# Performance work log

Hardware: AMD Instinct MI355X
Metric: run time of the kernel (lower is better)

The kernel has to match this reference:

```python
import jax, jax.numpy as jnp
import numpy as np

NUM_CLASSES = 80
ROI_SIZE = 7
SAMPLING = 2          # RoIAlign sampling_ratio
STRIDES = (4, 8, 16, 32)
FINEST_SCALE = 56.0
SCORE_THR = 0.05
IOU_THR = 0.5
MAX_PER_IMG = 100
MEANS = jnp.zeros((4,), jnp.float32)
STDS = jnp.array([0.1, 0.1, 0.2, 0.2], jnp.float32)
MAX_RATIO = abs(float(np.log(16.0 / 1000.0)))


def setup_inputs() -> dict:
    key = jax.random.key(0)
    ks = jax.random.split(key, 20)
    C, H0, W0 = 256, 200, 336
    inp = {}
    for i in range(4):
        inp[f"feat{i}"] = jax.random.normal(ks[i], (1, C, H0 >> i, W0 >> i), jnp.float32)
    N = 1000
    IMG_W, IMG_H = 1344.0, 800.0
    cx = jax.random.uniform(ks[4], (N,), minval=0.0, maxval=IMG_W)
    cy = jax.random.uniform(ks[5], (N,), minval=0.0, maxval=IMG_H)
    w = jax.random.uniform(ks[6], (N,), minval=16.0, maxval=512.0)
    h = jax.random.uniform(ks[7], (N,), minval=16.0, maxval=512.0)
    x1 = jnp.clip(cx - w / 2, 0.0, IMG_W - 1)
    y1 = jnp.clip(cy - h / 2, 0.0, IMG_H - 1)
    x2 = jnp.clip(cx + w / 2, x1 + 1.0, IMG_W)
    y2 = jnp.clip(cy + h / 2, y1 + 1.0, IMG_H)
    inp["proposals"] = jnp.stack([x1, y1, x2, y2], axis=-1)
    D = C * ROI_SIZE * ROI_SIZE  # 12544
    FC = 1024
    inp["fc1_w"] = 0.01 * jax.random.normal(ks[8], (FC, D), jnp.float32)
    inp["fc1_b"] = jnp.zeros((FC,), jnp.float32)
    inp["fc2_w"] = 0.01 * jax.random.normal(ks[9], (FC, FC), jnp.float32)
    inp["fc2_b"] = jnp.zeros((FC,), jnp.float32)
    inp["cls_w"] = 0.01 * jax.random.normal(ks[10], (NUM_CLASSES + 1, FC), jnp.float32)
    inp["cls_b"] = jnp.zeros((NUM_CLASSES + 1,), jnp.float32)
    inp["reg_w"] = 0.01 * jax.random.normal(ks[11], (NUM_CLASSES * 4, FC), jnp.float32)
    inp["reg_b"] = jnp.zeros((NUM_CLASSES * 4,), jnp.float32)
    return inp


def _roi_align(feat, rois, scale):
    # feat [C,H,W]; rois [N,4]; aligned RoIAlign, 7x7 out, sampling_ratio=2
    C, H, W = feat.shape
    P = ROI_SIZE * SAMPLING  # 14 uniform sample points per axis

    def one(roi):
        x1, y1, x2, y2 = roi[0], roi[1], roi[2], roi[3]
        sx = x1 * scale - 0.5
        sy = y1 * scale - 0.5
        rw = (x2 - x1) * scale
        rh = (y2 - y1) * scale
        pts = (jnp.arange(P, dtype=feat.dtype) + 0.5) / P
        xs = sx + pts * rw
        ys = sy + pts * rh
        y0 = jnp.floor(ys)
        x0 = jnp.floor(xs)
        ly = ys - y0
        lx = xs - x0
        y0i = jnp.clip(y0.astype(jnp.int32), 0, H - 1)
        y1i = jnp.clip(y0i + 1, 0, H - 1)
        x0i = jnp.clip(x0.astype(jnp.int32), 0, W - 1)
        x1i = jnp.clip(x0i + 1, 0, W - 1)
        g = lambda yi, xi: feat[:, yi[:, None], xi[None, :]]  # [C,P,P]
        ly_ = ly[None, :, None]
        lx_ = lx[None, None, :]
        val = (1 - ly_) * ((1 - lx_) * g(y0i, x0i) + lx_ * g(y0i, x1i)) \
            + ly_ * ((1 - lx_) * g(y1i, x0i) + lx_ * g(y1i, x1i))
        vy = ((ys >= -1.0) & (ys <= H))[None, :, None]
        vx = ((xs >= -1.0) & (xs <= W))[None, None, :]
        val = jnp.where(vy & vx, val, 0.0)
        # average-pool the 2x2 samples per bin -> [C,7,7]
        return val.reshape(C, ROI_SIZE, SAMPLING, ROI_SIZE, SAMPLING).mean(axis=(2, 4))

    return jax.vmap(one)(rois)  # [N,C,7,7]


def _delta2bbox(proposals, deltas):
    d = deltas.reshape(-1, NUM_CLASSES, 4) * STDS + MEANS
    dx, dy = d[..., 0], d[..., 1]
    dw = jnp.clip(d[..., 2], -MAX_RATIO, MAX_RATIO)
    dh = jnp.clip(d[..., 3], -MAX_RATIO, MAX_RATIO)
    px = ((proposals[:, 0] + proposals[:, 2]) * 0.5)[:, None]
    py = ((proposals[:, 1] + proposals[:, 3]) * 0.5)[:, None]
    pw = (proposals[:, 2] - proposals[:, 0])[:, None]
    ph = (proposals[:, 3] - proposals[:, 1])[:, None]
    gw = pw * jnp.exp(dw)
    gh = ph * jnp.exp(dh)
    gx = px + pw * dx
    gy = py + ph * dy
    return jnp.stack([gx - gw * 0.5, gy - gh * 0.5, gx + gw * 0.5, gy + gh * 0.5], axis=-1)


def _pairwise_iou(b):
    x1, y1, x2, y2 = b[:, 0], b[:, 1], b[:, 2], b[:, 3]
    area = jnp.maximum(x2 - x1, 0.0) * jnp.maximum(y2 - y1, 0.0)
    iw = jnp.maximum(jnp.minimum(x2[:, None], x2[None, :]) - jnp.maximum(x1[:, None], x1[None, :]), 0.0)
    ih = jnp.maximum(jnp.minimum(y2[:, None], y2[None, :]) - jnp.maximum(y1[:, None], y1[None, :]), 0.0)
    inter = iw * ih
    return inter / jnp.maximum(area[:, None] + area[None, :] - inter, 1e-8)


def _nms_one_class(boxes, scores):
    # greedy NMS, static shapes; returns score-sorted boxes/scores + keep mask
    N = scores.shape[0]
    order = jnp.argsort(-scores)
    b = boxes[order]
    s = scores[order]
    iou = _pairwise_iou(b)
    idx = jnp.arange(N)

    def body(i, keep):
        sup = (iou[i] > IOU_THR) & keep[i] & (idx > i)
        return keep & jnp.logical_not(sup)

    keep = jax.lax.fori_loop(0, N, body, s > SCORE_THR)
    return b, s, keep


def _batched_nms(bboxes, scores):
    # bboxes [N,81,4], scores [N,81]; class 80 is background (skipped)
    cls_boxes = jnp.transpose(bboxes[:, :NUM_CLASSES, :], (1, 0, 2))  # [80,N,4]
    cls_scores = scores[:, :NUM_CLASSES].T                            # [80,N]
    b, s, keep = jax.vmap(_nms_one_class)(cls_boxes, cls_scores)
    N = s.shape[1]
    s_flat = jnp.where(keep, s, -1.0).reshape(-1)
    topv, topi = jax.lax.top_k(s_flat, MAX_PER_IMG)
    det_boxes = b.reshape(-1, 4)[topi]
    det_classes = (topi // N).astype(jnp.int32)
    valid = topv > 0.0
    num_det = valid.sum().astype(jnp.int32)
    det_scores = jnp.where(valid, topv, 0.0)
    det_boxes = jnp.where(valid[:, None], det_boxes, 0.0)
    det_classes = jnp.where(valid, det_classes, -1)
    return num_det, det_boxes[None], det_scores[None], det_classes[None]


def _forward(feat0, feat1, feat2, feat3, proposals,
             fc1_w, fc1_b, fc2_w, fc2_b, cls_w, cls_b, reg_w, reg_b):
    feats = [feat0[0], feat1[0], feat2[0], feat3[0]]
    wp = proposals[:, 2] - proposals[:, 0]
    hp = proposals[:, 3] - proposals[:, 1]
    scale = jnp.sqrt(jnp.maximum(wp * hp, 1e-6))
    lvl = jnp.clip(jnp.floor(jnp.log2(scale / FINEST_SCALE + 1e-6)), 0, 3).astype(jnp.int32)
    N = proposals.shape[0]
    C = feats[0].shape[0]
    roi_feats = jnp.zeros((N, C, ROI_SIZE, ROI_SIZE), proposals.dtype)
    for l, stride in enumerate(STRIDES):
        f = _roi_align(feats[l], proposals, 1.0 / stride)
        roi_feats = jnp.where((lvl == l)[:, None, None, None], f, roi_feats)
    h = roi_feats.reshape(N, -1)
    h = jax.nn.relu(h @ fc1_w.T + fc1_b)
    h = jax.nn.relu(h @ fc2_w.T + fc2_b)
    cls_score = h @ cls_w.T + cls_b          # [N,81]
    bbox_pred = h @ reg_w.T + reg_b          # [N,320]
    scores = jax.nn.softmax(cls_score, axis=1)
    boxes = _delta2bbox(proposals, bbox_pred)                          # [N,80,4]
    boxes = jnp.concatenate([boxes, jnp.zeros((N, 1, 4), boxes.dtype)], axis=1)
    return _batched_nms(boxes, scores)


def reference(feat0, feat1, feat2, feat3, proposals,
              fc1_w, fc1_b, fc2_w, fc2_b, cls_w, cls_b, reg_w, reg_b):
    return _forward(feat0, feat1, feat2, feat3, proposals,
                    fc1_w, fc1_b, fc2_w, fc2_b, cls_w, cls_b, reg_w, reg_b)
```

## Files before the change

kernel.cpp:

```cpp
#include <hip/hip_runtime.h>
#include <math.h>

#define NCLS   80
#define NPROP  1000
#define FCDIM  1024
#define DFLAT  12544
#define MPAD   1024
#define MAXR   4.1351665567423560f
#define LDSP   40
#define NMSW   16
#define NCAT   404

#define CSPLIT 8
#define CG     (256 / CSPLIT)

typedef unsigned short ushort_t;
typedef unsigned long long ull_t;
using short8  = __attribute__((ext_vector_type(8))) short;
using float4v = __attribute__((ext_vector_type(4))) float;

__device__ inline ushort_t f2bf(float f) {
    unsigned int u = __float_as_uint(f);
    unsigned int r = (u + 0x7fffu + ((u >> 16) & 1u)) >> 16;
    return (ushort_t)r;
}

__device__ __forceinline__ unsigned cvtpk_bf16(float lo, float hi) {
    unsigned r;
    asm("v_cvt_pk_bf16_f32 %0, %1, %2" : "=v"(r) : "v"(lo), "v"(hi));
    return r;
}

__global__ __launch_bounds__(256) void roi_align_k(
    const float* __restrict__ f0, const float* __restrict__ f1,
    const float* __restrict__ f2, const float* __restrict__ f3,
    const float* __restrict__ props, ushort_t* __restrict__ Abf)
{
    int r  = blockIdx.x;
    int cz = blockIdx.y;
    int t  = threadIdx.x;

    if (r >= NPROP) {
        for (int i = t; i < CG * 49; i += 256)
            Abf[(size_t)r * DFLAT + cz * (CG * 49) + i] = 0;
        return;
    }

    const float4 p = *(const float4*)&props[(size_t)r * 4];
    float wp = p.z - p.x, hp = p.w - p.y;
    float scale = sqrtf(fmaxf(wp * hp, 1e-6f));
    int lvl = (int)floorf(log2f(scale / 56.0f + 1e-6f));
    lvl = min(max(lvl, 0), 3);

    const float* f; int H, W; float sc;
    switch (lvl) {
        case 0:  f = f0; H = 200; W = 336; sc = 0.25f;    break;
        case 1:  f = f1; H = 100; W = 168; sc = 0.125f;   break;
        case 2:  f = f2; H = 50;  W = 84;  sc = 0.0625f;  break;
        default: f = f3; H = 25;  W = 42;  sc = 0.03125f; break;
    }

    if (t >= 196) return;

    int b   = t >> 2;
    int sub = t & 3;
    int by = b / 7, bx = b - by * 7;
    int sy = by * 2 + (sub >> 1);
    int sx = bx * 2 + (sub & 1);

    float startx = p.x * sc - 0.5f, rangex = (p.z - p.x) * sc;
    float starty = p.y * sc - 0.5f, rangey = (p.w - p.y) * sc;
    float posx = startx + (((float)sx + 0.5f) / 14.0f) * rangex;
    float posy = starty + (((float)sy + 0.5f) / 14.0f) * rangey;

    float flx = floorf(posx), fly = floorf(posy);
    float lx = posx - flx, ly = posy - fly;
    int x0 = min(max((int)flx, 0), W - 1);
    int y0 = min(max((int)fly, 0), H - 1);
    int y1 = min(y0 + 1, H - 1);
    bool valid = (posx >= -1.0f) && (posx <= (float)W) &&
                 (posy >= -1.0f) && (posy <= (float)H);
    float vm = valid ? 0.25f : 0.0f;

    float w00 = (1.f - ly) * (1.f - lx) * vm;
    float w01 = (1.f - ly) * lx * vm;
    float w10 = ly * (1.f - lx) * vm;
    float w11 = ly * lx * vm;

    int  xb = min(x0, W - 2);
    bool xr = (x0 == W - 1);
    float wtA = xr ? 0.f : w00, wtB = xr ? (w00 + w01) : w01;
    float wbA = xr ? 0.f : w10, wbB = xr ? (w10 + w11) : w11;
    int ot = y0 * W + xb;
    int ob = y1 * W + xb;

    const int HW = H * W;
    ushort_t* orow = Abf + (size_t)r * DFLAT + cz * (CG * 49);
    const float* pl = f + (size_t)(cz * CG) * HW;

    #pragma unroll 8
    for (int c = 0; c < CG; c++) {
        float2 tv = *(const float2*)(pl + ot);
        float2 bv = *(const float2*)(pl + ob);
        float v = tv.x * wtA + tv.y * wtB + bv.x * wbA + bv.y * wbB;
        v += __shfl_xor(v, 1);
        v += __shfl_xor(v, 2);
        if (sub == 0)
            orow[c * 49 + b] = f2bf(v);
        pl += HW;
    }
}

__global__ __launch_bounds__(256) void gemm_sk_k(
    const ushort_t* __restrict__ A, const float* __restrict__ Wf,
    float* __restrict__ P, int N, int K, int KC)
{
    __shared__ ushort_t As[128 * LDSP];
    __shared__ ushort_t Bs[128 * LDSP];

    int tid = threadIdx.x;
    int w = tid >> 6, l = tid & 63;
    int wm = (w >> 1) * 64, wn = (w & 1) * 64;
    int m0 = blockIdx.y * 128, n0 = blockIdx.x * 128;
    int kc0 = blockIdx.z * KC;

    int lrow = tid >> 2;
    int lko  = (tid & 3) * 8;

    const ushort_t* Ag = A  + (size_t)(m0 + lrow) * K + kc0 + lko;
    const float*    Wg = Wf + (size_t)(n0 + lrow) * K + kc0 + lko;
    size_t rowK64 = (size_t)64 * K;

    float4v acc[4][4];
    #pragma unroll
    for (int i = 0; i < 4; i++)
        #pragma unroll
        for (int j = 0; j < 4; j++)
            acc[i][j] = (float4v){0.f, 0.f, 0.f, 0.f};

    int rl = l & 15, q = l >> 4;

    for (int k0 = 0; k0 < KC; k0 += 32) {
        uint4  a0  = *(const uint4*)(Ag + k0);
        uint4  a1  = *(const uint4*)(Ag + rowK64 + k0);
        float4 w0a = *(const float4*)(Wg + k0);
        float4 w0b = *(const float4*)(Wg + k0 + 4);
        float4 w1a = *(const float4*)(Wg + rowK64 + k0);
        float4 w1b = *(const float4*)(Wg + rowK64 + k0 + 4);

        uint4 wv0, wv1;
        wv0.x = cvtpk_bf16(w0a.x, w0a.y);
        wv0.y = cvtpk_bf16(w0a.z, w0a.w);
        wv0.z = cvtpk_bf16(w0b.x, w0b.y);
        wv0.w = cvtpk_bf16(w0b.z, w0b.w);
        wv1.x = cvtpk_bf16(w1a.x, w1a.y);
        wv1.y = cvtpk_bf16(w1a.z, w1a.w);
        wv1.z = cvtpk_bf16(w1b.x, w1b.y);
        wv1.w = cvtpk_bf16(w1b.z, w1b.w);

        *(uint4*)&As[lrow * LDSP + lko]        = a0;
        *(uint4*)&As[(lrow + 64) * LDSP + lko] = a1;
        *(uint4*)&Bs[lrow * LDSP + lko]        = wv0;
        *(uint4*)&Bs[(lrow + 64) * LDSP + lko] = wv1;
        __syncthreads();

        short8 af[4], bfr[4];
        #pragma unroll
        for (int i = 0; i < 4; i++)
            af[i] = *(const short8*)&As[(wm + i * 16 + rl) * LDSP + q * 8];
        #pragma unroll
        for (int j = 0; j < 4; j++)
            bfr[j] = *(const short8*)&Bs[(wn + j * 16 + rl) * LDSP + q * 8];

        #pragma unroll
        for (int i = 0; i < 4; i++)
            #pragma unroll
            for (int j = 0; j < 4; j++)
                acc[i][j] = __builtin_amdgcn_mfma_f32_16x16x32_bf16(
                    af[i], bfr[j], acc[i][j], 0, 0, 0);
        __syncthreads();
    }

    float* Pz = P + (size_t)blockIdx.z * ((size_t)MPAD * N);
    #pragma unroll
    for (int i = 0; i < 4; i++) {
        #pragma unroll
        for (int j = 0; j < 4; j++) {
            int col = n0 + wn + j * 16 + rl;
            #pragma unroll
            for (int rr = 0; rr < 4; rr++) {
                int row = m0 + wm + i * 16 + q * 4 + rr;
                Pz[(size_t)row * N + col] = acc[i][j][rr];
            }
        }
    }
}

__global__ __launch_bounds__(256) void reduce_sk_k(
    const float* __restrict__ P, const float* __restrict__ bias,
    void* __restrict__ Cout, int N, int SK, int relu, int out_bf16)
{
    size_t idx = ((size_t)blockIdx.x * 256 + threadIdx.x) * 4;
    float4 s = *(const float4*)&P[idx];
    for (int z = 1; z < SK; z++) {
        float4 pv = *(const float4*)&P[(size_t)z * ((size_t)MPAD * N) + idx];
        s.x += pv.x; s.y += pv.y; s.z += pv.z; s.w += pv.w;
    }
    int n = (int)(idx % N);
    float4 b = *(const float4*)&bias[n];
    s.x += b.x; s.y += b.y; s.z += b.z; s.w += b.w;
    if (relu) {
        s.x = fmaxf(s.x, 0.f); s.y = fmaxf(s.y, 0.f);
        s.z = fmaxf(s.z, 0.f); s.w = fmaxf(s.w, 0.f);
    }
    if (out_bf16) {
        ushort4 o;
        o.x = f2bf(s.x); o.y = f2bf(s.y); o.z = f2bf(s.z); o.w = f2bf(s.w);
        *(ushort4*)&((ushort_t*)Cout)[idx] = o;
    } else {
        *(float4*)&((float*)Cout)[idx] = s;
    }
}

__global__ __launch_bounds__(256) void concat_w_k(
    const float* __restrict__ reg_w, const float* __restrict__ cls_w,
    const float* __restrict__ reg_b, const float* __restrict__ cls_b,
    float* __restrict__ Wcat, float* __restrict__ bcat)
{
    int row = blockIdx.x;
    int t = threadIdx.x;
    float4 v = make_float4(0.f, 0.f, 0.f, 0.f);
    float bv = 0.f;
    if (row < 320) {
        v = *(const float4*)&reg_w[(size_t)row * FCDIM + t * 4];
        bv = reg_b[row];
    } else if (row < NCAT - 3) {
        v = *(const float4*)&cls_w[(size_t)(row - 320) * FCDIM + t * 4];
        bv = cls_b[row - 320];
    }
    *(float4*)&Wcat[(size_t)row * FCDIM + t * 4] = v;
    if (t == 0) bcat[row] = bv;
}

__global__ __launch_bounds__(256) void gemm_tn_k(
    const float* __restrict__ A, const float* __restrict__ W,
    const float* __restrict__ bias, float* __restrict__ C,
    int M, int N, int K, int relu)
{
    __shared__ float As[16][64];
    __shared__ float Bs[16][64];

    int tid = threadIdx.x;
    int tx = tid & 15;
    int ty = tid >> 4;
    int m0 = blockIdx.y * 64, n0 = blockIdx.x * 64;

    int lr = tid >> 2;
    int lk = (tid & 3) << 2;

    const float* Arow = A + (size_t)(m0 + lr) * K + lk;
    const float* Wrow = W + (size_t)(n0 + lr) * K + lk;
    bool mOK = (m0 + lr) < M;
    bool nOK = (n0 + lr) < N;

    float acc[4][4] = {};

    for (int k0 = 0; k0 < K; k0 += 16) {
        float4 av = mOK ? *(const float4*)(Arow + k0) : make_float4(0.f, 0.f, 0.f, 0.f);
        float4 wv = nOK ? *(const float4*)(Wrow + k0) : make_float4(0.f, 0.f, 0.f, 0.f);
        As[lk + 0][lr] = av.x; As[lk + 1][lr] = av.y;
        As[lk + 2][lr] = av.z; As[lk + 3][lr] = av.w;
        Bs[lk + 0][lr] = wv.x; Bs[lk + 1][lr] = wv.y;
        Bs[lk + 2][lr] = wv.z; Bs[lk + 3][lr] = wv.w;
        __syncthreads();

        #pragma unroll
        for (int kk = 0; kk < 16; kk++) {
            float4 a = *(const float4*)&As[kk][ty << 2];
            float4 b = *(const float4*)&Bs[kk][tx << 2];
            acc[0][0] += a.x * b.x; acc[0][1] += a.x * b.y;
            acc[0][2] += a.x * b.z; acc[0][3] += a.x * b.w;
            acc[1][0] += a.y * b.x; acc[1][1] += a.y * b.y;
            acc[1][2] += a.y * b.z; acc[1][3] += a.y * b.w;
            acc[2][0] += a.z * b.x; acc[2][1] += a.z * b.y;
            acc[2][2] += a.z * b.z; acc[2][3] += a.z * b.w;
            acc[3][0] += a.w * b.x; acc[3][1] += a.w * b.y;
            acc[3][2] += a.w * b.z; acc[3][3] += a.w * b.w;
        }
        __syncthreads();
    }

    #pragma unroll
    for (int i = 0; i < 4; i++) {
        int m = m0 + (ty << 2) + i;
        if (m >= M) continue;
        #pragma unroll
        for (int j = 0; j < 4; j++) {
            int n = n0 + (tx << 2) + j;
            if (n < N) {
                float v = acc[i][j] + bias[n];
                if (relu) v = fmaxf(v, 0.f);
                C[(size_t)m * N + n] = v;
            }
        }
    }
}

__global__ __launch_bounds__(128) void head_post_k(
    const float* __restrict__ hr_s, const float* __restrict__ props,
    float* __restrict__ probsT, float* __restrict__ boxesT)
{
    int r = blockIdx.x, t = threadIdx.x;
    __shared__ float red[128];

    float x = (t < 81) ? hr_s[(size_t)r * NCAT + 320 + t] : -1e30f;
    red[t] = x; __syncthreads();
    for (int s = 64; s > 0; s >>= 1) {
        if (t < s) red[t] = fmaxf(red[t], red[t + s]);
        __syncthreads();
    }
    float mx = red[0];
    __syncthreads();

    float e = (t < 81) ? expf(x - mx) : 0.f;
    red[t] = e; __syncthreads();
    for (int s = 64; s > 0; s >>= 1) {
        if (t < s) red[t] += red[t + s];
        __syncthreads();
    }
    float inv = 1.f / red[0];

    if (t < NCLS) {
        probsT[(size_t)t * NPROP + r] = e * inv;

        const float4 p = *(const float4*)&props[(size_t)r * 4];
        float4 d = *(const float4*)&hr_s[(size_t)r * NCAT + t * 4];
        float dx = d.x * 0.1f, dy = d.y * 0.1f;
        float dw = fminf(fmaxf(d.z * 0.2f, -MAXR), MAXR);
        float dh = fminf(fmaxf(d.w * 0.2f, -MAXR), MAXR);
        float px = (p.x + p.z) * 0.5f, py = (p.y + p.w) * 0.5f;
        float pw = p.z - p.x, ph = p.w - p.y;
        float gw = pw * expf(dw), gh = ph * expf(dh);
        float gx = px + pw * dx, gy = py + ph * dy;
        float4 bo = make_float4(gx - gw * 0.5f, gy - gh * 0.5f,
                                gx + gw * 0.5f, gy + gh * 0.5f);
        *(float4*)&boxesT[(size_t)(t * NPROP + r) * 4] = bo;
    }
}

__global__ __launch_bounds__(512) void sort_k(
    const float* __restrict__ probsT, const float* __restrict__ boxesT,
    float* __restrict__ sortedS, float* __restrict__ sortedB)
{
    int c = blockIdx.x, t = threadIdx.x;
    __shared__ float sk[1024];
    __shared__ int   si[1024];

    for (int j = t; j < 1024; j += 512) {
        sk[j] = (j < NPROP) ? probsT[(size_t)c * NPROP + j] : -1e30f;
        si[j] = j;
    }
    __syncthreads();

    for (int size = 2; size <= 1024; size <<= 1) {
        for (int stride = size >> 1; stride > 0; stride >>= 1) {
            int i = (t << 1) - (t & (stride - 1));
            int j = i + stride;
            float ka = sk[i], kb = sk[j];
            int ia = si[i], ib = si[j];
            bool aFirst = (ka > kb) || (ka == kb && ia < ib);
            bool desc = ((i & size) == 0);
            if (desc ? !aFirst : aFirst) {
                sk[i] = kb; sk[j] = ka; si[i] = ib; si[j] = ia;
            }
            __syncthreads();
        }
    }

    for (int j = t; j < NPROP; j += 512) {
        sortedS[(size_t)c * NPROP + j] = sk[j];
        const float4 bb = *(const float4*)&boxesT[(size_t)(c * NPROP + si[j]) * 4];
        *(float4*)&sortedB[(size_t)(c * NPROP + j) * 4] = bb;
    }
}

__global__ __launch_bounds__(256) void nms_mask_k(
    const float* __restrict__ sortedS, const float* __restrict__ sortedB,
    ull_t* __restrict__ masks)
{
    int c = blockIdx.x;
    int i = blockIdx.y * 256 + threadIdx.x;
    __shared__ float x1s[NPROP], y1s[NPROP], x2s[NPROP], y2s[NPROP], ars[NPROP];

    for (int j = threadIdx.x; j < NPROP; j += 256) {
        float4 b = *(const float4*)&sortedB[(size_t)(c * NPROP + j) * 4];
        x1s[j] = b.x; y1s[j] = b.y; x2s[j] = b.z; y2s[j] = b.w;
        ars[j] = fmaxf(b.z - b.x, 0.f) * fmaxf(b.w - b.y, 0.f);
    }
    __syncthreads();

    if (i >= NPROP) return;
    if (!(sortedS[(size_t)c * NPROP + i] > 0.05f)) return;

    float xi1 = x1s[i], yi1 = y1s[i], xi2 = x2s[i], yi2 = y2s[i], ai = ars[i];
    ull_t* row = masks + ((size_t)c * NPROP + i) * NMSW;

    for (int w = 0; w < NMSW; w++) {
        ull_t m = 0ull;
        int j0 = w << 6;
        #pragma unroll 4
        for (int k = 0; k < 64; k++) {
            int j = j0 + k;
            if (j < NPROP) {
                float iw = fmaxf(fminf(xi2, x2s[j]) - fmaxf(xi1, x1s[j]), 0.f);
                float ih = fmaxf(fminf(yi2, y2s[j]) - fmaxf(yi1, y1s[j]), 0.f);
                float inter = iw * ih;
                float iou = inter / fmaxf(ai + ars[j] - inter, 1e-8f);
                if (iou > 0.5f) m |= (1ull << k);
            }
        }
        row[w] = m;
    }
}

__global__ __launch_bounds__(256) void nms_scan_k(
    const float* __restrict__ sortedS, const ull_t* __restrict__ masks,
    float* __restrict__ candS, int* __restrict__ candI)
{
    int c = blockIdx.x, t = threadIdx.x;
    __shared__ unsigned char kp[NPROP];
    __shared__ int segc[256];

    for (int j = t; j < NPROP; j += 256)
        kp[j] = sortedS[(size_t)c * NPROP + j] > 0.05f ? 1 : 0;
    __syncthreads();

    if (t < 64) {
        const ull_t* M = masks + (size_t)c * NPROP * NMSW;
        ull_t rem = 0ull;
        for (int i = 0; i < NPROP; i++) {
            if (kp[i]) {
                ull_t w = __shfl(rem, i >> 6);
                if ((w >> (i & 63)) & 1ull) {
                    if (t == 0) kp[i] = 0;
                } else {
                    if (t < NMSW) rem |= M[(size_t)i * NMSW + t];
                }
            }
        }
    }
    __syncthreads();

    int j0 = t * 4;
    int cnt = 0;
    #pragma unroll
    for (int k = 0; k < 4; k++) {
        int j = j0 + k;
        if (j < NPROP && kp[j]) cnt++;
    }
    segc[t] = cnt;
    __syncthreads();
    for (int off = 1; off < 256; off <<= 1) {
        int add = (t >= off) ? segc[t - off] : 0;
        __syncthreads();
        segc[t] += add;
        __syncthreads();
    }
    int pos = segc[t] - cnt;
    #pragma unroll
    for (int k = 0; k < 4; k++) {
        int j = j0 + k;
        if (j < NPROP && kp[j]) {
            if (pos < 100) {
                candS[c * 100 + pos] = sortedS[(size_t)c * NPROP + j];
                candI[c * 100 + pos] = c * NPROP + j;
            }
            pos++;
        }
    }
    int total = segc[255];
    for (int p = total + t; p < 100; p += 256) {
        candS[c * 100 + p] = -2e30f;
        candI[c * 100 + p] = 0x7fffffff;
    }
}

__global__ __launch_bounds__(128) void merge_k(
    const float* __restrict__ candS, const int* __restrict__ candI,
    const float* __restrict__ sortedB, float* __restrict__ out)
{
    int t = threadIdx.x;
    __shared__ int   head[NCLS];
    __shared__ float topv[100];
    __shared__ int   topi[100];

    if (t < NCLS) head[t] = 0;
    __syncthreads();

    for (int r = 0; r < 100; r++) {
        if (t < 64) {
            float v = -2e30f; int fi = 0x7fffffff; int cls = 0;
            {
                int h = head[t];
                if (h < 100) { v = candS[t * 100 + h]; fi = candI[t * 100 + h]; cls = t; }
            }
            int c2 = t + 64;
            if (c2 < NCLS) {
                int h = head[c2];
                if (h < 100) {
                    float v2 = candS[c2 * 100 + h]; int fi2 = candI[c2 * 100 + h];
                    if (v2 > v || (v2 == v && fi2 < fi)) { v = v2; fi = fi2; cls = c2; }
                }
            }
            #pragma unroll
            for (int s = 1; s < 64; s <<= 1) {
                float ov = __shfl_xor(v, s);
                int ofi  = __shfl_xor(fi, s);
                int ocl  = __shfl_xor(cls, s);
                if (ov > v || (ov == v && ofi < fi)) { v = ov; fi = ofi; cls = ocl; }
            }
            if (t == 0) { topv[r] = v; topi[r] = fi; head[cls]++; }
        }
        __syncthreads();
    }

    if (t < 100) {
        float v = topv[t]; int fi = topi[t];
        bool valid = v > 0.0f;
        float4 bb = make_float4(0.f, 0.f, 0.f, 0.f);
        if (valid) bb = *(const float4*)&sortedB[(size_t)fi * 4];
        out[1 + t * 4 + 0] = bb.x;
        out[1 + t * 4 + 1] = bb.y;
        out[1 + t * 4 + 2] = bb.z;
        out[1 + t * 4 + 3] = bb.w;
        out[401 + t] = valid ? v : 0.0f;
        out[501 + t] = valid ? (float)(fi / NPROP) : -1.0f;
    }
    if (t == 0) {
        int n = 0;
        for (int r = 0; r < 100; r++) n += (topv[r] > 0.0f) ? 1 : 0;
        out[0] = (float)n;
    }
}

extern "C" void kernel_launch(void* const* d_in, const int* in_sizes, int n_in,
                              void* d_out, int out_size, void* d_ws, size_t ws_size,
                              hipStream_t stream)
{
    const float* f0    = (const float*)d_in[0];
    const float* f1    = (const float*)d_in[1];
    const float* f2    = (const float*)d_in[2];
    const float* f3    = (const float*)d_in[3];
    const float* props = (const float*)d_in[4];
    const float* fc1_w = (const float*)d_in[5];
    const float* fc1_b = (const float*)d_in[6];
    const float* fc2_w = (const float*)d_in[7];
    const float* fc2_b = (const float*)d_in[8];
    const float* cls_w = (const float*)d_in[9];
    const float* cls_b = (const float*)d_in[10];
    const float* reg_w = (const float*)d_in[11];
    const float* reg_b = (const float*)d_in[12];
    float* out = (float*)d_out;

    unsigned char* base = (unsigned char*)d_ws;
    ushort_t* Abf  = (ushort_t*)(base);
    ushort_t* h1   = (ushort_t*)(base + 25690112);
    float*    P1   = (float*)(base + 27787264);
    float*    P2   = (float*)(base + 27787264);
    float*    h2   = (float*)(base + 44564480);
    float*    hr_s    = (float*)(base + 48758784);
    float*    probsT  = (float*)(base + 50401280);
    float*    boxesT  = (float*)(base + 50721280);
    float*    sortedS = (float*)(base + 52001280);
    float*    sortedB = (float*)(base + 52321280);
    float*    candS   = (float*)(base + 53601280);
    int*      candI   = (int*)(base + 53633280);
    float*    Wcat    = (float*)(base + 53665280);
    float*    bcat    = (float*)(base + 55320064);
    ull_t*    masks   = (ull_t*)(base);

    roi_align_k<<<dim3(MPAD, CSPLIT), 256, 0, stream>>>(f0, f1, f2, f3, props, Abf);

    gemm_sk_k<<<dim3(FCDIM / 128, MPAD / 128, 8), 256, 0, stream>>>(
        Abf, fc1_w, P1, FCDIM, DFLAT, DFLAT / 8);
    reduce_sk_k<<<(MPAD * FCDIM / 4) / 256, 256, 0, stream>>>(
        P1, fc1_b, h1, FCDIM, 8, 1, 1);

    concat_w_k<<<NCAT, 256, 0, stream>>>(reg_w, cls_w, reg_b, cls_b, Wcat, bcat);

    gemm_sk_k<<<dim3(FCDIM / 128, MPAD / 128, 4), 256, 0, stream>>>(
        h1, fc2_w, P2, FCDIM, FCDIM, FCDIM / 4);
    reduce_sk_k<<<(MPAD * FCDIM / 4) / 256, 256, 0, stream>>>(
        P2, fc2_b, h2, FCDIM, 4, 1, 0);

    gemm_tn_k<<<dim3((NCAT + 63) / 64, (NPROP + 63) / 64), 256, 0, stream>>>(
        h2, Wcat, bcat, hr_s, NPROP, NCAT, FCDIM, 0);

    head_post_k<<<NPROP, 128, 0, stream>>>(hr_s, props, probsT, boxesT);
    sort_k<<<NCLS, 512, 0, stream>>>(probsT, boxesT, sortedS, sortedB);
    nms_mask_k<<<dim3(NCLS, (NPROP + 255) / 256), 256, 0, stream>>>(
        sortedS, sortedB, masks);
    nms_scan_k<<<NCLS, 256, 0, stream>>>(sortedS, masks, candS, candI);
    merge_k<<<1, 128, 0, stream>>>(candS, candI, sortedB, out);
}
```

Before: 572.7 us.

## Double-buffer split-K GEMM LDS, remap block order, fuse NMS mask and scan

The split-K GEMM now double-buffers its LDS tiles, loading and converting the next K-slice from global memory while the MFMAs run on the current one. This halves the barriers per iteration and hides load latency. Block indices are remapped from a linear id so that consecutive blocks share the same M/K slice, which should improve L2 reuse of A and W. Separately, the NMS mask and scan kernels are fused into one per-class kernel, removing a launch, but mask computation now uses only 80 blocks instead of 320, reducing parallelism.

Measured after the change: 565.9 us. Within noise of the previous version (-1.2%).

```diff
diff --git a/kernel.cpp b/kernel.cpp
--- a/kernel.cpp
+++ b/kernel.cpp
@@ -115,14 +115,21 @@
     const ushort_t* __restrict__ A, const float* __restrict__ Wf,
     float* __restrict__ P, int N, int K, int KC)
 {
-    __shared__ ushort_t As[128 * LDSP];
-    __shared__ ushort_t Bs[128 * LDSP];
+    __shared__ ushort_t As[2][128 * LDSP];
+    __shared__ ushort_t Bs[2][128 * LDSP];
 
     int tid = threadIdx.x;
     int w = tid >> 6, l = tid & 63;
     int wm = (w >> 1) * 64, wn = (w & 1) * 64;
-    int m0 = blockIdx.y * 128, n0 = blockIdx.x * 128;
-    int kc0 = blockIdx.z * KC;
+
+    int bid = (int)blockIdx.x + (int)gridDim.x * ((int)blockIdx.y + (int)gridDim.y * (int)blockIdx.z);
+    int bx = bid & 7;
+    int slot = bid >> 3;
+    int by = slot % (int)gridDim.y;
+    int bz = slot / (int)gridDim.y;
+
+    int m0 = by * 128, n0 = bx * 128;
+    int kc0 = bz * KC;
 
     int lrow = tid >> 2;
     int lko  = (tid & 3) * 8;
@@ -140,37 +147,49 @@
 
     int rl = l & 15, q = l >> 4;
 
+    {
+        uint4  a0  = *(const uint4*)(Ag);
+        uint4  a1  = *(const uint4*)(Ag + rowK64);
+        float4 w0a = *(const float4*)(Wg);
+        float4 w0b = *(const float4*)(Wg + 4);
+        float4 w1a = *(const float4*)(Wg + rowK64);
+        float4 w1b = *(const float4*)(Wg + rowK64 + 4);
+        uint4 wv0, wv1;
+        wv0.x = cvtpk_bf16(w0a.x, w0a.y); wv0.y = cvtpk_bf16(w0a.z, w0a.w);
+        wv0.z = cvtpk_bf16(w0b.x, w0b.y); wv0.w = cvtpk_bf16(w0b.z, w0b.w);
+        wv1.x = cvtpk_bf16(w1a.x, w1a.y); wv1.y = cvtpk_bf16(w1a.z, w1a.w);
+        wv1.z = cvtpk_bf16(w1b.x, w1b.y); wv1.w = cvtpk_bf16(w1b.z, w1b.w);
+        *(uint4*)&As[0][lrow * LDSP + lko]        = a0;
+        *(uint4*)&As[0][(lrow + 64) * LDSP + lko] = a1;
+        *(uint4*)&Bs[0][lrow * LDSP + lko]        = wv0;
+        *(uint4*)&Bs[0][(lrow + 64) * LDSP + lko] = wv1;
+    }
+    __syncthreads();
+
+    int cur = 0;
     for (int k0 = 0; k0 < KC; k0 += 32) {
-        uint4  a0  = *(const uint4*)(Ag + k0);
-        uint4  a1  = *(const uint4*)(Ag + rowK64 + k0);
-        float4 w0a = *(const float4*)(Wg + k0);
-        float4 w0b = *(const float4*)(Wg + k0 + 4);
-        float4 w1a = *(const float4*)(Wg + rowK64 + k0);
-        float4 w1b = *(const float4*)(Wg + rowK64 + k0 + 4);
-
-        uint4 wv0, wv1;
-        wv0.x = cvtpk_bf16(w0a.x, w0a.y);
-        wv0.y = cvtpk_bf16(w0a.z, w0a.w);
-        wv0.z = cvtpk_bf16(w0b.x, w0b.y);
-        wv0.w = cvtpk_bf16(w0b.z, w0b.w);
-        wv1.x = cvtpk_bf16(w1a.x, w1a.y);
-        wv1.y = cvtpk_bf16(w1a.z, w1a.w);
-        wv1.z = cvtpk_bf16(w1b.x, w1b.y);
-        wv1.w = cvtpk_bf16(w1b.z, w1b.w);
-
-        *(uint4*)&As[lrow * LDSP + lko]        = a0;
-        *(uint4*)&As[(lrow + 64) * LDSP + lko] = a1;
-        *(uint4*)&Bs[lrow * LDSP + lko]        = wv0;
-        *(uint4*)&Bs[(lrow + 64) * LDSP + lko] = wv1;
-        __syncthreads();
-
+        bool more = (k0 + 32) < KC;
+
+        uint4 na0, na1;
+        float4 nw0a, nw0b, nw1a, nw1b;
+        if (more) {
+            na0  = *(const uint4*)(Ag + k0 + 32);
+            na1  = *(const uint4*)(Ag + rowK64 + k0 + 32);
+            nw0a = *(const float4*)(Wg + k0 + 32);
+            nw0b = *(const float4*)(Wg + k0 + 36);
+            nw1a = *(const float4*)(Wg + rowK64 + k0 + 32);
+            nw1b = *(const float4*)(Wg + rowK64 + k0 + 36);
+        }
+
+        const ushort_t* Ac = As[cur];
+        const ushort_t* Bc = Bs[cur];
         short8 af[4], bfr[4];
         #pragma unroll
         for (int i = 0; i < 4; i++)
-            af[i] = *(const short8*)&As[(wm + i * 16 + rl) * LDSP + q * 8];
+            af[i] = *(const short8*)&Ac[(wm + i * 16 + rl) * LDSP + q * 8];
         #pragma unroll
         for (int j = 0; j < 4; j++)
-            bfr[j] = *(const short8*)&Bs[(wn + j * 16 + rl) * LDSP + q * 8];
+            bfr[j] = *(const short8*)&Bc[(wn + j * 16 + rl) * LDSP + q * 8];
 
         #pragma unroll
         for (int i = 0; i < 4; i++)
@@ -178,10 +197,26 @@
             for (int j = 0; j < 4; j++)
                 acc[i][j] = __builtin_amdgcn_mfma_f32_16x16x32_bf16(
                     af[i], bfr[j], acc[i][j], 0, 0, 0);
-        __syncthreads();
-    }
-
-    float* Pz = P + (size_t)blockIdx.z * ((size_t)MPAD * N);
+
+        if (more) {
+            uint4 wv0, wv1;
+            wv0.x = cvtpk_bf16(nw0a.x, nw0a.y); wv0.y = cvtpk_bf16(nw0a.z, nw0a.w);
+            wv0.z = cvtpk_bf16(nw0b.x, nw0b.y); wv0.w = cvtpk_bf16(nw0b.z, nw0b.w);
+            wv1.x = cvtpk_bf16(nw1a.x, nw1a.y); wv1.y = cvtpk_bf16(nw1a.z, nw1a.w);
+            wv1.z = cvtpk_bf16(nw1b.x, nw1b.y); wv1.w = cvtpk_bf16(nw1b.z, nw1b.w);
+            ushort_t* An = As[cur ^ 1];
+            ushort_t* Bn = Bs[cur ^ 1];
+            *(uint4*)&An[lrow * LDSP + lko]        = na0;
+            *(uint4*)&An[(lrow + 64) * LDSP + lko] = na1;
+            *(uint4*)&Bn[lrow * LDSP + lko]        = wv0;
+            *(uint4*)&Bn[(lrow + 64) * LDSP + lko] = wv1;
+        }
+
+        __syncthreads();
+        cur ^= 1;
+    }
+
+    float* Pz = P + (size_t)bz * ((size_t)MPAD * N);
     #pragma unroll
     for (int i = 0; i < 4; i++) {
         #pragma unroll
@@ -384,59 +419,47 @@
     }
 }
 
-__global__ __launch_bounds__(256) void nms_mask_k(
+__global__ __launch_bounds__(256) void nms_k(
     const float* __restrict__ sortedS, const float* __restrict__ sortedB,
-    ull_t* __restrict__ masks)
-{
-    int c = blockIdx.x;
-    int i = blockIdx.y * 256 + threadIdx.x;
+    ull_t* __restrict__ masks, float* __restrict__ candS, int* __restrict__ candI)
+{
+    int c = blockIdx.x, t = threadIdx.x;
     __shared__ float x1s[NPROP], y1s[NPROP], x2s[NPROP], y2s[NPROP], ars[NPROP];
-
-    for (int j = threadIdx.x; j < NPROP; j += 256) {
+    __shared__ unsigned char kp[NPROP];
+    __shared__ int segc[256];
+
+    for (int j = t; j < NPROP; j += 256) {
         float4 b = *(const float4*)&sortedB[(size_t)(c * NPROP + j) * 4];
         x1s[j] = b.x; y1s[j] = b.y; x2s[j] = b.z; y2s[j] = b.w;
         ars[j] = fmaxf(b.z - b.x, 0.f) * fmaxf(b.w - b.y, 0.f);
-    }
-    __syncthreads();
-
-    if (i >= NPROP) return;
-    if (!(sortedS[(size_t)c * NPROP + i] > 0.05f)) return;
-
-    float xi1 = x1s[i], yi1 = y1s[i], xi2 = x2s[i], yi2 = y2s[i], ai = ars[i];
-    ull_t* row = masks + ((size_t)c * NPROP + i) * NMSW;
-
-    for (int w = 0; w < NMSW; w++) {
-        ull_t m = 0ull;
-        int j0 = w << 6;
-        #pragma unroll 4
-        for (int k = 0; k < 64; k++) {
-            int j = j0 + k;
-            if (j < NPROP) {
-                float iw = fmaxf(fminf(xi2, x2s[j]) - fmaxf(xi1, x1s[j]), 0.f);
-                float ih = fmaxf(fminf(yi2, y2s[j]) - fmaxf(yi1, y1s[j]), 0.f);
-                float inter = iw * ih;
-                float iou = inter / fmaxf(ai + ars[j] - inter, 1e-8f);
-                if (iou > 0.5f) m |= (1ull << k);
-            }
-        }
-        row[w] = m;
-    }
-}
-
-__global__ __launch_bounds__(256) void nms_scan_k(
-    const float* __restrict__ sortedS, const ull_t* __restrict__ masks,
-    float* __restrict__ candS, int* __restrict__ candI)
-{
-    int c = blockIdx.x, t = threadIdx.x;
-    __shared__ unsigned char kp[NPROP];
-    __shared__ int segc[256];
-
-    for (int j = t; j < NPROP; j += 256)
         kp[j] = sortedS[(size_t)c * NPROP + j] > 0.05f ? 1 : 0;
+    }
+    __syncthreads();
+
+    ull_t* M = masks + (size_t)c * NPROP * NMSW;
+    for (int i = t; i < NPROP; i += 256) {
+        if (!kp[i]) continue;
+        float xi1 = x1s[i], yi1 = y1s[i], xi2 = x2s[i], yi2 = y2s[i], ai = ars[i];
+        for (int w = 0; w < NMSW; w++) {
+            ull_t m = 0ull;
+            int j0 = w << 6;
+            #pragma unroll 4
+            for (int k = 0; k < 64; k++) {
+                int j = j0 + k;
+                if (j < NPROP) {
+                    float iw = fmaxf(fminf(xi2, x2s[j]) - fmaxf(xi1, x1s[j]), 0.f);
+                    float ih = fmaxf(fminf(yi2, y2s[j]) - fmaxf(yi1, y1s[j]), 0.f);
+                    float inter = iw * ih;
+                    float iou = inter / fmaxf(ai + ars[j] - inter, 1e-8f);
+                    if (iou > 0.5f) m |= (1ull << k);
+                }
+            }
+            M[(size_t)i * NMSW + w] = m;
+        }
+    }
     __syncthreads();
 
     if (t < 64) {
-        const ull_t* M = masks + (size_t)c * NPROP * NMSW;
         ull_t rem = 0ull;
         for (int i = 0; i < NPROP; i++) {
             if (kp[i]) {
@@ -598,8 +621,6 @@
 
     head_post_k<<<NPROP, 128, 0, stream>>>(hr_s, props, probsT, boxesT);
     sort_k<<<NCLS, 512, 0, stream>>>(probsT, boxesT, sortedS, sortedB);
-    nms_mask_k<<<dim3(NCLS, (NPROP + 255) / 256), 256, 0, stream>>>(
-        sortedS, sortedB, masks);
-    nms_scan_k<<<NCLS, 256, 0, stream>>>(sortedS, masks, candS, candI);
+    nms_k<<<NCLS, 256, 0, stream>>>(sortedS, sortedB, masks, candS, candI);
     merge_k<<<1, 128, 0, stream>>>(candS, candI, sortedB, out);
 }
```
